# Optimization experiments

Measured on AMD Instinct MI355X. Metric: run time of the kernel, lower is better.

Reference implementation:

```python
import jax, jax.numpy as jnp
import numpy as np

D_MODEL = 256
NUM_UNIVERSES = 8
D_UNIVERSE = D_MODEL // NUM_UNIVERSES
B, S = 1, 1024
TEMP = 5.0
NEG = -1e9


def setup_inputs() -> dict:
    key = jax.random.key(0)
    ks = jax.random.split(key, 5)
    scale = 1.0 / np.sqrt(D_MODEL)
    return {
        "x": jax.random.normal(ks[0], (B, S, D_MODEL), dtype=jnp.float32),
        "Wq": jax.random.normal(ks[1], (D_MODEL, D_MODEL), dtype=jnp.float32) * scale,
        "bq": jnp.zeros((D_MODEL,), dtype=jnp.float32),
        "Wk": jax.random.normal(ks[2], (D_MODEL, D_MODEL), dtype=jnp.float32) * scale,
        "bk": jnp.zeros((D_MODEL,), dtype=jnp.float32),
        "Wv": jax.random.normal(ks[3], (D_MODEL, D_MODEL), dtype=jnp.float32) * scale,
        "bv": jnp.zeros((D_MODEL,), dtype=jnp.float32),
        "Wo": jax.random.normal(ks[4], (D_MODEL, D_MODEL), dtype=jnp.float32) * scale,
        "bo": jnp.zeros((D_MODEL,), dtype=jnp.float32),
    }


def reference(x, Wq, bq, Wk, bk, Wv, bv, Wo, bo):
    b, s, d = x.shape
    h, du = NUM_UNIVERSES, D_UNIVERSE
    # Projections; Q,K squashed to [0,1] fuzzy truth values
    Q = jax.nn.sigmoid(x @ Wq + bq)
    K = jax.nn.sigmoid(x @ Wk + bk)
    V = x @ Wv + bv
    # [B,S,D] -> [B,H,S,du]
    Q = Q.reshape(b, s, h, du).transpose(0, 2, 1, 3)
    K = K.reshape(b, s, h, du).transpose(0, 2, 1, 3)
    V = V.reshape(b, s, h, du).transpose(0, 2, 1, 3)
    # Fuzzy implication: clamp(1 - Q_i + K_j, max=1), mean over d_universe
    # Broadcast to [B,H,S,S,du] (the memory-heavy intermediate)
    implication = jnp.minimum(1.0 - Q[:, :, :, None, :] + K[:, :, None, :, :], 1.0)
    truth = implication.mean(axis=-1)  # [B,H,S,S]
    # Causal mask
    causal = jnp.tril(jnp.ones((s, s), dtype=bool))
    truth = jnp.where(causal[None, None], truth, NEG)
    attn = jax.nn.softmax(truth * TEMP, axis=-1)
    out = jnp.einsum("bhij,bhjd->bhid", attn, V)
    out = out.transpose(0, 2, 1, 3).reshape(b, s, d)
    return out @ Wo + bo
```

## Files before the change

### kernel.cpp

```cpp
#include <hip/hip_runtime.h>
#include <hip/hip_bf16.h>
#include <math.h>

#define S_LEN 1024
#define DM    256
#define DU    32
#define TEMPF 5.0f
#define NS    4

typedef float    f32x4  __attribute__((ext_vector_type(4)));
typedef short    bf16x8 __attribute__((ext_vector_type(8)));
typedef _Float16 f16x2  __attribute__((ext_vector_type(2)));
typedef _Float16 f16x8  __attribute__((ext_vector_type(8)));

__device__ __forceinline__ unsigned short f32_to_bf16_rne(float x) {
    unsigned int b = __float_as_uint(x);
    b += 0x7FFFu + ((b >> 16) & 1u);
    return (unsigned short)(b >> 16);
}

__device__ __forceinline__ void split_bf16(float f, unsigned short& h, unsigned short& l) {
    h = f32_to_bf16_rne(f);
    float hf = __uint_as_float((unsigned int)h << 16);
    l = f32_to_bf16_rne(f - hf);
}

__global__ __launch_bounds__(256) void qkv_proj_kernel(
    const float* __restrict__ x,
    const float* __restrict__ Wq, const float* __restrict__ bq,
    const float* __restrict__ Wk, const float* __restrict__ bk,
    const float* __restrict__ Wv, const float* __restrict__ bv,
    float* __restrict__ qo, float* __restrict__ ko, float* __restrict__ vo)
{
    const int n0g = blockIdx.x * 64;
    const int mat = n0g >> 8;
    const int n0  = n0g & 255;
    const float* __restrict__ W    = (mat == 0) ? Wq : ((mat == 1) ? Wk : Wv);
    const float* __restrict__ bias = (mat == 0) ? bq : ((mat == 1) ? bk : bv);
    float* __restrict__ dst        = (mat == 0) ? qo : ((mat == 1) ? ko : vo);

    const int m0   = blockIdx.y * 64;
    const int t    = threadIdx.x;
    const int w    = t >> 6;
    const int lane = t & 63;
    const int fm   = lane & 15;
    const int quad = lane >> 4;
    const int q8   = quad * 8;

    __shared__ __align__(16) unsigned short Ah[2][64][40], Al[2][64][40];
    __shared__ __align__(16) unsigned short Bh[2][64][40], Bl[2][64][40];

    const int xr  = t >> 2;
    const int xf  = (t & 3) * 8;
    const int wn  = t & 63;
    const int wkc = (t >> 6) * 8;

    f32x4 acc[4];
    #pragma unroll
    for (int nt = 0; nt < 4; nt++)
        #pragma unroll
        for (int i = 0; i < 4; i++) acc[nt][i] = 0.0f;

    const float* xbase = x + (m0 + xr) * DM + xf;
    float xa[8], wv[8];

    {
        float4 a0 = *(const float4*)xbase;
        float4 a1 = *(const float4*)(xbase + 4);
        xa[0]=a0.x; xa[1]=a0.y; xa[2]=a0.z; xa[3]=a0.w;
        xa[4]=a1.x; xa[5]=a1.y; xa[6]=a1.z; xa[7]=a1.w;
        #pragma unroll
        for (int i = 0; i < 8; i++) wv[i] = W[(wkc + i) * DM + n0 + wn];
    }
    {
        bf16x8 vh, vl;
        #pragma unroll
        for (int i = 0; i < 8; i++) { unsigned short h,l; split_bf16(xa[i],h,l); vh[i]=(short)h; vl[i]=(short)l; }
        *(bf16x8*)&Ah[0][xr][xf] = vh; *(bf16x8*)&Al[0][xr][xf] = vl;
        #pragma unroll
        for (int i = 0; i < 8; i++) { unsigned short h,l; split_bf16(wv[i],h,l); vh[i]=(short)h; vl[i]=(short)l; }
        *(bf16x8*)&Bh[0][wn][wkc] = vh; *(bf16x8*)&Bl[0][wn][wkc] = vl;
    }
    __syncthreads();

    int buf = 0;
    for (int step = 0; step < 8; step++) {
        if (step < 7) {
            const float* xp = xbase + (step + 1) * 32;
            float4 a0 = *(const float4*)xp;
            float4 a1 = *(const float4*)(xp + 4);
            xa[0]=a0.x; xa[1]=a0.y; xa[2]=a0.z; xa[3]=a0.w;
            xa[4]=a1.x; xa[5]=a1.y; xa[6]=a1.z; xa[7]=a1.w;
            #pragma unroll
            for (int i = 0; i < 8; i++)
                wv[i] = W[((step + 1) * 32 + wkc + i) * DM + n0 + wn];
        }
        {
            bf16x8 ah = *(const bf16x8*)&Ah[buf][16 * w + fm][q8];
            bf16x8 al = *(const bf16x8*)&Al[buf][16 * w + fm][q8];
            #pragma unroll
            for (int nt = 0; nt < 4; nt++) {
                bf16x8 bh = *(const bf16x8*)&Bh[buf][nt * 16 + fm][q8];
                bf16x8 bl = *(const bf16x8*)&Bl[buf][nt * 16 + fm][q8];
                acc[nt] = __builtin_amdgcn_mfma_f32_16x16x32_bf16(ah, bh, acc[nt], 0, 0, 0);
                acc[nt] = __builtin_amdgcn_mfma_f32_16x16x32_bf16(al, bh, acc[nt], 0, 0, 0);
                acc[nt] = __builtin_amdgcn_mfma_f32_16x16x32_bf16(ah, bl, acc[nt], 0, 0, 0);
            }
        }
        if (step < 7) {
            const int nb = buf ^ 1;
            bf16x8 vh, vl;
            #pragma unroll
            for (int i = 0; i < 8; i++) { unsigned short h,l; split_bf16(xa[i],h,l); vh[i]=(short)h; vl[i]=(short)l; }
            *(bf16x8*)&Ah[nb][xr][xf] = vh; *(bf16x8*)&Al[nb][xr][xf] = vl;
            #pragma unroll
            for (int i = 0; i < 8; i++) { unsigned short h,l; split_bf16(wv[i],h,l); vh[i]=(short)h; vl[i]=(short)l; }
            *(bf16x8*)&Bh[nb][wn][wkc] = vh; *(bf16x8*)&Bl[nb][wn][wkc] = vl;
            __syncthreads();
            buf = nb;
        }
    }

    #pragma unroll
    for (int nt = 0; nt < 4; nt++) {
        const int col = n0 + nt * 16 + fm;
        const float bb = bias[col];
        const int hh = col >> 5;
        const int dd = col & 31;
        float* dp = dst + hh * (S_LEN * DU) + dd;
        #pragma unroll
        for (int reg = 0; reg < 4; reg++) {
            const int row = m0 + 16 * w + quad * 4 + reg;
            float val = acc[nt][reg] + bb;
            if (mat < 2) val = 1.0f / (1.0f + __expf(-val));
            dp[row * DU] = val;
        }
    }
}

__global__ __launch_bounds__(256, 2) void attn_kernel(
    const float* __restrict__ q, const float* __restrict__ k,
    const float* __restrict__ v,
    float* __restrict__ part_o, float* __restrict__ part_l)
{
    const int bid = blockIdx.x;
    const int it4 = 15 - (bid >> 5);
    const int sub = bid & 31;
    const int h   = sub & 7;
    const int s   = sub >> 3;
    const int t   = threadIdx.x;
    const int r   = t >> 4;
    const int c   = t & 15;
    const int w   = t >> 6;
    const int i0  = it4 * 64;

    __shared__ __align__(16) _Float16       Kh[64][40];
    __shared__ __align__(16) unsigned short Vt[32][88];
    __shared__ __align__(16) unsigned short Ps[64][88];

    f16x2 qh[4][16];
    #pragma unroll
    for (int kq = 0; kq < 4; kq++) {
        const float* qrow = q + h * (S_LEN * DU) + (i0 + r + 16 * kq) * DU;
        #pragma unroll
        for (int d4 = 0; d4 < 8; d4++) {
            float4 qv = *(const float4*)&qrow[d4 * 4];
            qh[kq][d4*2+0] = (f16x2){(_Float16)qv.x, (_Float16)qv.y};
            qh[kq][d4*2+1] = (f16x2){(_Float16)qv.z, (_Float16)qv.w};
        }
    }
    const f16x2 one2  = {(_Float16)1.0f, (_Float16)1.0f};
    const f16x2 zero2 = {(_Float16)0.0f, (_Float16)0.0f};

    float lpart[4] = {0.0f, 0.0f, 0.0f, 0.0f};
    f32x4 acc0 = {0.0f, 0.0f, 0.0f, 0.0f};
    f32x4 acc1 = {0.0f, 0.0f, 0.0f, 0.0f};

    const int jr = t >> 2;
    const int d0 = (t & 3) * 8;
    const float* kbase = k + h * (S_LEN * DU);
    const float* vbase = v + h * (S_LEN * DU);

    const int lane = t & 63;
    const int m    = lane & 15;
    const int quad = lane >> 4;

    const int njt = it4 + 1;
    float4 ka, kb, va, vb;
    if (s < njt) {
        const float* kp = kbase + (s * 64 + jr) * DU + d0;
        const float* vp = vbase + (s * 64 + jr) * DU + d0;
        ka = *(const float4*)kp; kb = *(const float4*)(kp + 4);
        va = *(const float4*)vp; vb = *(const float4*)(vp + 4);
    }

    for (int jt = s; jt < njt; jt += NS) {
        __syncthreads();
        {
            float kv[8] = {ka.x, ka.y, ka.z, ka.w, kb.x, kb.y, kb.z, kb.w};
            f16x8 kh8;
            #pragma unroll
            for (int i = 0; i < 8; i++) kh8[i] = (_Float16)kv[i];
            *(f16x8*)&Kh[jr][d0] = kh8;
            float vv[8] = {va.x, va.y, va.z, va.w, vb.x, vb.y, vb.z, vb.w};
            #pragma unroll
            for (int i = 0; i < 8; i++)
                Vt[d0 + i][jr] = f32_to_bf16_rne(vv[i]);
        }
        __syncthreads();
        if (jt + NS < njt) {
            const float* kp = kbase + ((jt + NS) * 64 + jr) * DU + d0;
            const float* vp = vbase + ((jt + NS) * 64 + jr) * DU + d0;
            ka = *(const float4*)kp; kb = *(const float4*)(kp + 4);
            va = *(const float4*)vp; vb = *(const float4*)(vp + 4);
        }

        #pragma unroll
        for (int q4 = 0; q4 < 4; q4++) {
            const int jj  = c + q4 * 16;
            const int jgl = jt * 64 + jj;
            float sacc[4] = {0.0f, 0.0f, 0.0f, 0.0f};
            #pragma unroll
            for (int d8 = 0; d8 < 4; d8++) {
                f16x8 k8 = *(const f16x8*)&Kh[jj][d8 * 8];
                #pragma unroll
                for (int p2 = 0; p2 < 4; p2++) {
                    f16x2 kk = {k8[2*p2], k8[2*p2+1]};
                    #pragma unroll
                    for (int kq = 0; kq < 4; kq++) {
                        f16x2 diff = qh[kq][d8*4+p2] - kk;
                        f16x2 mx = __builtin_elementwise_max(diff, zero2);
#if defined(__has_builtin) && __has_builtin(__builtin_amdgcn_fdot2)
                        sacc[kq] = __builtin_amdgcn_fdot2(mx, one2, sacc[kq], false);
#else
                        sacc[kq] += (float)mx[0] + (float)mx[1];
#endif
                    }
                }
            }
            #pragma unroll
            for (int kq = 0; kq < 4; kq++) {
                const int ig = i0 + r + 16 * kq;
                const float p = (jgl <= ig)
                    ? __expf(TEMPF - (TEMPF / 32.0f) * sacc[kq]) : 0.0f;
                lpart[kq] += p;
                Ps[r + 16 * kq][jj] = f32_to_bf16_rne(p);
            }
        }
        __syncthreads();

        #pragma unroll
        for (int kc = 0; kc < 2; kc++) {
            bf16x8 a  = *(const bf16x8*)&Ps[16 * w + m][kc * 32 + quad * 8];
            bf16x8 b0 = *(const bf16x8*)&Vt[m]     [kc * 32 + quad * 8];
            bf16x8 b1 = *(const bf16x8*)&Vt[m + 16][kc * 32 + quad * 8];
            acc0 = __builtin_amdgcn_mfma_f32_16x16x32_bf16(a, b0, acc0, 0, 0, 0);
            acc1 = __builtin_amdgcn_mfma_f32_16x16x32_bf16(a, b1, acc1, 0, 0, 0);
        }
    }

    #pragma unroll
    for (int off = 8; off; off >>= 1)
        #pragma unroll
        for (int kq = 0; kq < 4; kq++)
            lpart[kq] += __shfl_xor(lpart[kq], off, 16);

    const int pbase = (h * 16 + it4) * NS + s;
    float* po = part_o + (size_t)pbase * 2048;
    #pragma unroll
    for (int reg = 0; reg < 4; reg++) {
        const int row = 16 * w + quad * 4 + reg;
        po[row * 32 + m]      = acc0[reg];
        po[row * 32 + m + 16] = acc1[reg];
    }
    if (c == 0) {
        #pragma unroll
        for (int kq = 0; kq < 4; kq++)
            part_l[pbase * 64 + r + 16 * kq] = lpart[kq];
    }
}

__global__ __launch_bounds__(256) void out_proj_kernel(
    const float* __restrict__ part_o, const float* __restrict__ part_l,
    const float* __restrict__ W, const float* __restrict__ bias,
    float* __restrict__ dst)
{
    const int n0  = blockIdx.x * 32;
    const int it4 = blockIdx.y;
    const int m0  = it4 * 64;
    const int t    = threadIdx.x;
    const int w    = t >> 6;
    const int lane = t & 63;
    const int fm   = lane & 15;
    const int quad = lane >> 4;
    const int q8   = quad * 8;

    __shared__ __align__(16) unsigned short Ah[2][64][40], Al[2][64][40];
    __shared__ __align__(16) unsigned short Bh[2][32][40], Bl[2][32][40];

    const int xr  = t >> 2;
    const int xf  = (t & 3) * 8;
    const int wn  = t & 31;
    const int wkb = (t >> 5) * 4;

    f32x4 acc[2];
    #pragma unroll
    for (int nt = 0; nt < 2; nt++)
        #pragma unroll
        for (int i = 0; i < 4; i++) acc[nt][i] = 0.0f;

    float xa[8], wv[4];

    auto loadA = [&](int h) {
        const int base = (h * 16 + it4) * NS;
        float o[8] = {0,0,0,0,0,0,0,0};
        float l = 0.0f;
        #pragma unroll
        for (int s2 = 0; s2 < NS; s2++) {
            const float* po = part_o + (size_t)(base + s2) * 2048 + xr * 32 + xf;
            float4 p0 = *(const float4*)po;
            float4 p1 = *(const float4*)(po + 4);
            o[0]+=p0.x; o[1]+=p0.y; o[2]+=p0.z; o[3]+=p0.w;
            o[4]+=p1.x; o[5]+=p1.y; o[6]+=p1.z; o[7]+=p1.w;
            l += part_l[(base + s2) * 64 + xr];
        }
        const float inv = 1.0f / l;
        #pragma unroll
        for (int i = 0; i < 8; i++) xa[i] = o[i] * inv;
    };
    auto loadW = [&](int k0) {
        #pragma unroll
        for (int i = 0; i < 4; i++) wv[i] = W[(k0 + wkb + i) * DM + n0 + wn];
    };
    auto storeT = [&](int b) {
        bf16x8 vh, vl;
        #pragma unroll
        for (int i = 0; i < 8; i++) { unsigned short h,l; split_bf16(xa[i],h,l); vh[i]=(short)h; vl[i]=(short)l; }
        *(bf16x8*)&Ah[b][xr][xf] = vh; *(bf16x8*)&Al[b][xr][xf] = vl;
        ushort4 bh4, bl4;
        unsigned short hh, ll;
        split_bf16(wv[0], hh, ll); bh4.x = hh; bl4.x = ll;
        split_bf16(wv[1], hh, ll); bh4.y = hh; bl4.y = ll;
        split_bf16(wv[2], hh, ll); bh4.z = hh; bl4.z = ll;
        split_bf16(wv[3], hh, ll); bh4.w = hh; bl4.w = ll;
        *(ushort4*)&Bh[b][wn][wkb] = bh4;
        *(ushort4*)&Bl[b][wn][wkb] = bl4;
    };

    loadA(0); loadW(0);
    storeT(0);
    __syncthreads();

    int buf = 0;
    for (int step = 0; step < 8; step++) {
        if (step < 7) { loadA(step + 1); loadW((step + 1) * 32); }
        {
            bf16x8 ah = *(const bf16x8*)&Ah[buf][16 * w + fm][q8];
            bf16x8 al = *(const bf16x8*)&Al[buf][16 * w + fm][q8];
            #pragma unroll
            for (int nt = 0; nt < 2; nt++) {
                bf16x8 bh = *(const bf16x8*)&Bh[buf][nt * 16 + fm][q8];
                bf16x8 bl = *(const bf16x8*)&Bl[buf][nt * 16 + fm][q8];
                acc[nt] = __builtin_amdgcn_mfma_f32_16x16x32_bf16(ah, bh, acc[nt], 0, 0, 0);
                acc[nt] = __builtin_amdgcn_mfma_f32_16x16x32_bf16(al, bh, acc[nt], 0, 0, 0);
                acc[nt] = __builtin_amdgcn_mfma_f32_16x16x32_bf16(ah, bl, acc[nt], 0, 0, 0);
            }
        }
        if (step < 7) {
            const int nb = buf ^ 1;
            storeT(nb);
            __syncthreads();
            buf = nb;
        }
    }

    #pragma unroll
    for (int nt = 0; nt < 2; nt++) {
        const int col = n0 + nt * 16 + fm;
        const float bb = bias[col];
        #pragma unroll
        for (int reg = 0; reg < 4; reg++) {
            const int row = m0 + 16 * w + quad * 4 + reg;
            dst[row * DM + col] = acc[nt][reg] + bb;
        }
    }
}

extern "C" void kernel_launch(void* const* d_in, const int* in_sizes, int n_in,
                              void* d_out, int out_size, void* d_ws, size_t ws_size,
                              hipStream_t stream)
{
    const float* x  = (const float*)d_in[0];
    const float* Wq = (const float*)d_in[1];
    const float* bq = (const float*)d_in[2];
    const float* Wk = (const float*)d_in[3];
    const float* bk = (const float*)d_in[4];
    const float* Wv = (const float*)d_in[5];
    const float* bv = (const float*)d_in[6];
    const float* Wo = (const float*)d_in[7];
    const float* bo = (const float*)d_in[8];
    float* out = (float*)d_out;

    float* ws      = (float*)d_ws;
    float* q       = ws;
    float* k       = q + 262144;
    float* v       = k + 262144;
    float* part_o  = v + 262144;
    float* part_l  = part_o + 1048576;

    qkv_proj_kernel<<<dim3(12, 16), 256, 0, stream>>>(x, Wq, bq, Wk, bk, Wv, bv, q, k, v);
    attn_kernel<<<dim3(512), 256, 0, stream>>>(q, k, v, part_o, part_l);
    out_proj_kernel<<<dim3(8, 16), 256, 0, stream>>>(part_o, part_l, Wo, bo, out);
}
```

Measured before the change: 107.1 us.

## Rebalance causal attention split-K and halve projection tiles for more blocks

The attention kernel now splits long causal row tiles (it4 >= 8) across 8 KV-splits instead of 4, so the grid grows from 512 to 768 blocks and the longest blocks get shorter, and occupancy is raised to 3 blocks per CU. The QKV and output projection kernels use 32-row tiles, doubling their block counts so more CUs have work. The output reduction reads a variable number of partials per row tile, and the workspace for partials grows. The trade-off is more partial writes and reduction traffic plus smaller per-block MFMA work.

```diff
diff --git a/kernel.cpp b/kernel.cpp
--- a/kernel.cpp
+++ b/kernel.cpp
@@ -6,13 +6,15 @@
 #define DM    256
 #define DU    32
 #define TEMPF 5.0f
-#define NS    4
 
 typedef float    f32x4  __attribute__((ext_vector_type(4)));
 typedef short    bf16x8 __attribute__((ext_vector_type(8)));
 typedef _Float16 f16x2  __attribute__((ext_vector_type(2)));
 typedef _Float16 f16x8  __attribute__((ext_vector_type(8)));
 
+__device__ __host__ inline int task_cnt(int it4)  { return it4 < 8 ? 4 : 8; }
+__device__ __host__ inline int task_base(int it4) { return it4 < 8 ? it4 * 4 : 32 + (it4 - 8) * 8; }
+
 __device__ __forceinline__ unsigned short f32_to_bf16_rne(float x) {
     unsigned int b = __float_as_uint(x);
     b += 0x7FFFu + ((b >> 16) & 1u);
@@ -25,7 +27,7 @@
     l = f32_to_bf16_rne(f - hf);
 }
 
-__global__ __launch_bounds__(256) void qkv_proj_kernel(
+__global__ __launch_bounds__(256, 2) void qkv_proj_kernel(
     const float* __restrict__ x,
     const float* __restrict__ Wq, const float* __restrict__ bq,
     const float* __restrict__ Wk, const float* __restrict__ bk,
@@ -39,69 +41,70 @@
     const float* __restrict__ bias = (mat == 0) ? bq : ((mat == 1) ? bk : bv);
     float* __restrict__ dst        = (mat == 0) ? qo : ((mat == 1) ? ko : vo);
 
-    const int m0   = blockIdx.y * 64;
+    const int m0   = blockIdx.y * 32;
     const int t    = threadIdx.x;
     const int w    = t >> 6;
     const int lane = t & 63;
     const int fm   = lane & 15;
     const int quad = lane >> 4;
     const int q8   = quad * 8;
-
-    __shared__ __align__(16) unsigned short Ah[2][64][40], Al[2][64][40];
+    const int mh   = w & 1;
+    const int nb2  = (w >> 1) * 2;
+
+    __shared__ __align__(16) unsigned short Ah[2][32][40], Al[2][32][40];
     __shared__ __align__(16) unsigned short Bh[2][64][40], Bl[2][64][40];
 
-    const int xr  = t >> 2;
-    const int xf  = (t & 3) * 8;
+    const int xr  = t >> 3;
+    const int xf  = (t & 7) * 4;
     const int wn  = t & 63;
     const int wkc = (t >> 6) * 8;
 
-    f32x4 acc[4];
+    f32x4 acc[2];
     #pragma unroll
-    for (int nt = 0; nt < 4; nt++)
+    for (int nt = 0; nt < 2; nt++)
         #pragma unroll
         for (int i = 0; i < 4; i++) acc[nt][i] = 0.0f;
 
     const float* xbase = x + (m0 + xr) * DM + xf;
-    float xa[8], wv[8];
-
-    {
-        float4 a0 = *(const float4*)xbase;
-        float4 a1 = *(const float4*)(xbase + 4);
+    float xa[4], wv[8];
+
+    auto loadX = [&](int k0) {
+        float4 a0 = *(const float4*)(xbase + k0);
         xa[0]=a0.x; xa[1]=a0.y; xa[2]=a0.z; xa[3]=a0.w;
-        xa[4]=a1.x; xa[5]=a1.y; xa[6]=a1.z; xa[7]=a1.w;
-        #pragma unroll
-        for (int i = 0; i < 8; i++) wv[i] = W[(wkc + i) * DM + n0 + wn];
-    }
-    {
+    };
+    auto loadW = [&](int k0) {
+        #pragma unroll
+        for (int i = 0; i < 8; i++) wv[i] = W[(k0 + wkc + i) * DM + n0 + wn];
+    };
+    auto storeT = [&](int b) {
+        ushort4 ah4, al4;
+        unsigned short hh, ll;
+        split_bf16(xa[0], hh, ll); ah4.x = hh; al4.x = ll;
+        split_bf16(xa[1], hh, ll); ah4.y = hh; al4.y = ll;
+        split_bf16(xa[2], hh, ll); ah4.z = hh; al4.z = ll;
+        split_bf16(xa[3], hh, ll); ah4.w = hh; al4.w = ll;
+        *(ushort4*)&Ah[b][xr][xf] = ah4;
+        *(ushort4*)&Al[b][xr][xf] = al4;
         bf16x8 vh, vl;
         #pragma unroll
-        for (int i = 0; i < 8; i++) { unsigned short h,l; split_bf16(xa[i],h,l); vh[i]=(short)h; vl[i]=(short)l; }
-        *(bf16x8*)&Ah[0][xr][xf] = vh; *(bf16x8*)&Al[0][xr][xf] = vl;
-        #pragma unroll
-        for (int i = 0; i < 8; i++) { unsigned short h,l; split_bf16(wv[i],h,l); vh[i]=(short)h; vl[i]=(short)l; }
-        *(bf16x8*)&Bh[0][wn][wkc] = vh; *(bf16x8*)&Bl[0][wn][wkc] = vl;
-    }
+        for (int i = 0; i < 8; i++) { unsigned short h2,l2; split_bf16(wv[i],h2,l2); vh[i]=(short)h2; vl[i]=(short)l2; }
+        *(bf16x8*)&Bh[b][wn][wkc] = vh; *(bf16x8*)&Bl[b][wn][wkc] = vl;
+    };
+
+    loadX(0); loadW(0);
+    storeT(0);
     __syncthreads();
 
     int buf = 0;
     for (int step = 0; step < 8; step++) {
-        if (step < 7) {
-            const float* xp = xbase + (step + 1) * 32;
-            float4 a0 = *(const float4*)xp;
-            float4 a1 = *(const float4*)(xp + 4);
-            xa[0]=a0.x; xa[1]=a0.y; xa[2]=a0.z; xa[3]=a0.w;
-            xa[4]=a1.x; xa[5]=a1.y; xa[6]=a1.z; xa[7]=a1.w;
+        if (step < 7) { loadX((step + 1) * 32); loadW((step + 1) * 32); }
+        {
+            bf16x8 ah = *(const bf16x8*)&Ah[buf][16 * mh + fm][q8];
+            bf16x8 al = *(const bf16x8*)&Al[buf][16 * mh + fm][q8];
             #pragma unroll
-            for (int i = 0; i < 8; i++)
-                wv[i] = W[((step + 1) * 32 + wkc + i) * DM + n0 + wn];
-        }
-        {
-            bf16x8 ah = *(const bf16x8*)&Ah[buf][16 * w + fm][q8];
-            bf16x8 al = *(const bf16x8*)&Al[buf][16 * w + fm][q8];
-            #pragma unroll
-            for (int nt = 0; nt < 4; nt++) {
-                bf16x8 bh = *(const bf16x8*)&Bh[buf][nt * 16 + fm][q8];
-                bf16x8 bl = *(const bf16x8*)&Bl[buf][nt * 16 + fm][q8];
+            for (int nt = 0; nt < 2; nt++) {
+                bf16x8 bh = *(const bf16x8*)&Bh[buf][(nb2 + nt) * 16 + fm][q8];
+                bf16x8 bl = *(const bf16x8*)&Bl[buf][(nb2 + nt) * 16 + fm][q8];
                 acc[nt] = __builtin_amdgcn_mfma_f32_16x16x32_bf16(ah, bh, acc[nt], 0, 0, 0);
                 acc[nt] = __builtin_amdgcn_mfma_f32_16x16x32_bf16(al, bh, acc[nt], 0, 0, 0);
                 acc[nt] = __builtin_amdgcn_mfma_f32_16x16x32_bf16(ah, bl, acc[nt], 0, 0, 0);
@@ -109,28 +112,22 @@
         }
         if (step < 7) {
             const int nb = buf ^ 1;
-            bf16x8 vh, vl;
-            #pragma unroll
-            for (int i = 0; i < 8; i++) { unsigned short h,l; split_bf16(xa[i],h,l); vh[i]=(short)h; vl[i]=(short)l; }
-            *(bf16x8*)&Ah[nb][xr][xf] = vh; *(bf16x8*)&Al[nb][xr][xf] = vl;
-            #pragma unroll
-            for (int i = 0; i < 8; i++) { unsigned short h,l; split_bf16(wv[i],h,l); vh[i]=(short)h; vl[i]=(short)l; }
-            *(bf16x8*)&Bh[nb][wn][wkc] = vh; *(bf16x8*)&Bl[nb][wn][wkc] = vl;
+            storeT(nb);
             __syncthreads();
             buf = nb;
         }
     }
 
     #pragma unroll
-    for (int nt = 0; nt < 4; nt++) {
-        const int col = n0 + nt * 16 + fm;
+    for (int nt = 0; nt < 2; nt++) {
+        const int col = n0 + (nb2 + nt) * 16 + fm;
         const float bb = bias[col];
         const int hh = col >> 5;
         const int dd = col & 31;
         float* dp = dst + hh * (S_LEN * DU) + dd;
         #pragma unroll
         for (int reg = 0; reg < 4; reg++) {
-            const int row = m0 + 16 * w + quad * 4 + reg;
+            const int row = m0 + 16 * mh + quad * 4 + reg;
             float val = acc[nt][reg] + bb;
             if (mat < 2) val = 1.0f / (1.0f + __expf(-val));
             dp[row * DU] = val;
@@ -138,16 +135,17 @@
     }
 }
 
-__global__ __launch_bounds__(256, 2) void attn_kernel(
+__global__ __launch_bounds__(256, 3) void attn_kernel(
     const float* __restrict__ q, const float* __restrict__ k,
     const float* __restrict__ v,
     float* __restrict__ part_o, float* __restrict__ part_l)
 {
     const int bid = blockIdx.x;
-    const int it4 = 15 - (bid >> 5);
-    const int sub = bid & 31;
-    const int h   = sub & 7;
-    const int s   = sub >> 3;
+    const int h   = bid / 96;
+    const int rm  = bid - h * 96;
+    int it4, s, NSi;
+    if (rm < 32) { it4 = rm >> 2;        s = rm & 3;         NSi = 4; }
+    else         { it4 = 8 + ((rm - 32) >> 3); s = (rm - 32) & 7; NSi = 8; }
     const int t   = threadIdx.x;
     const int r   = t >> 4;
     const int c   = t & 15;
@@ -194,7 +192,7 @@
         va = *(const float4*)vp; vb = *(const float4*)(vp + 4);
     }
 
-    for (int jt = s; jt < njt; jt += NS) {
+    for (int jt = s; jt < njt; jt += NSi) {
         __syncthreads();
         {
             float kv[8] = {ka.x, ka.y, ka.z, ka.w, kb.x, kb.y, kb.z, kb.w};
@@ -208,9 +206,9 @@
                 Vt[d0 + i][jr] = f32_to_bf16_rne(vv[i]);
         }
         __syncthreads();
-        if (jt + NS < njt) {
-            const float* kp = kbase + ((jt + NS) * 64 + jr) * DU + d0;
-            const float* vp = vbase + ((jt + NS) * 64 + jr) * DU + d0;
+        if (jt + NSi < njt) {
+            const float* kp = kbase + ((jt + NSi) * 64 + jr) * DU + d0;
+            const float* vp = vbase + ((jt + NSi) * 64 + jr) * DU + d0;
             ka = *(const float4*)kp; kb = *(const float4*)(kp + 4);
             va = *(const float4*)vp; vb = *(const float4*)(vp + 4);
         }
@@ -265,7 +263,7 @@
         for (int kq = 0; kq < 4; kq++)
             lpart[kq] += __shfl_xor(lpart[kq], off, 16);
 
-    const int pbase = (h * 16 + it4) * NS + s;
+    const int pbase = h * 96 + task_base(it4) + s;
     float* po = part_o + (size_t)pbase * 2048;
     #pragma unroll
     for (int reg = 0; reg < 4; reg++) {
@@ -280,71 +278,71 @@
     }
 }
 
-__global__ __launch_bounds__(256) void out_proj_kernel(
+__global__ __launch_bounds__(256, 2) void out_proj_kernel(
     const float* __restrict__ part_o, const float* __restrict__ part_l,
     const float* __restrict__ W, const float* __restrict__ bias,
     float* __restrict__ dst)
 {
-    const int n0  = blockIdx.x * 32;
-    const int it4 = blockIdx.y;
-    const int m0  = it4 * 64;
+    const int n0   = blockIdx.x * 32;
+    const int m0   = blockIdx.y * 32;
+    const int it4  = m0 >> 6;
+    const int half = m0 & 32;
     const int t    = threadIdx.x;
     const int w    = t >> 6;
     const int lane = t & 63;
     const int fm   = lane & 15;
     const int quad = lane >> 4;
     const int q8   = quad * 8;
-
-    __shared__ __align__(16) unsigned short Ah[2][64][40], Al[2][64][40];
+    const int mh   = w & 1;
+    const int nh   = w >> 1;
+
+    __shared__ __align__(16) unsigned short Ah[2][32][40], Al[2][32][40];
     __shared__ __align__(16) unsigned short Bh[2][32][40], Bl[2][32][40];
 
-    const int xr  = t >> 2;
-    const int xf  = (t & 3) * 8;
+    const int xr  = t >> 3;
+    const int xf  = (t & 7) * 4;
     const int wn  = t & 31;
     const int wkb = (t >> 5) * 4;
 
-    f32x4 acc[2];
-    #pragma unroll
-    for (int nt = 0; nt < 2; nt++)
-        #pragma unroll
-        for (int i = 0; i < 4; i++) acc[nt][i] = 0.0f;
-
-    float xa[8], wv[4];
+    f32x4 acc = {0.0f, 0.0f, 0.0f, 0.0f};
+    float xa[4], wv[4];
+
+    const int cnt  = task_cnt(it4);
+    const int tb   = task_base(it4);
 
     auto loadA = [&](int h) {
-        const int base = (h * 16 + it4) * NS;
-        float o[8] = {0,0,0,0,0,0,0,0};
+        const int base = h * 96 + tb;
+        float o[4] = {0,0,0,0};
         float l = 0.0f;
-        #pragma unroll
-        for (int s2 = 0; s2 < NS; s2++) {
-            const float* po = part_o + (size_t)(base + s2) * 2048 + xr * 32 + xf;
+        for (int s2 = 0; s2 < cnt; s2++) {
+            const float* po = part_o + (size_t)(base + s2) * 2048 + (half + xr) * 32 + xf;
             float4 p0 = *(const float4*)po;
-            float4 p1 = *(const float4*)(po + 4);
             o[0]+=p0.x; o[1]+=p0.y; o[2]+=p0.z; o[3]+=p0.w;
-            o[4]+=p1.x; o[5]+=p1.y; o[6]+=p1.z; o[7]+=p1.w;
-            l += part_l[(base + s2) * 64 + xr];
+            l += part_l[(base + s2) * 64 + half + xr];
         }
         const float inv = 1.0f / l;
         #pragma unroll
-        for (int i = 0; i < 8; i++) xa[i] = o[i] * inv;
+        for (int i = 0; i < 4; i++) xa[i] = o[i] * inv;
     };
     auto loadW = [&](int k0) {
         #pragma unroll
         for (int i = 0; i < 4; i++) wv[i] = W[(k0 + wkb + i) * DM + n0 + wn];
     };
     auto storeT = [&](int b) {
-        bf16x8 vh, vl;
-        #pragma unroll
-        for (int i = 0; i < 8; i++) { unsigned short h,l; split_bf16(xa[i],h,l); vh[i]=(short)h; vl[i]=(short)l; }
-        *(bf16x8*)&Ah[b][xr][xf] = vh; *(bf16x8*)&Al[b][xr][xf] = vl;
-        ushort4 bh4, bl4;
+        ushort4 h4, l4;
         unsigned short hh, ll;
-        split_bf16(wv[0], hh, ll); bh4.x = hh; bl4.x = ll;
-        split_bf16(wv[1], hh, ll); bh4.y = hh; bl4.y = ll;
-        split_bf16(wv[2], hh, ll); bh4.z = hh; bl4.z = ll;
-        split_bf16(wv[3], hh, ll); bh4.w = hh; bl4.w = ll;
-        *(ushort4*)&Bh[b][wn][wkb] = bh4;
-        *(ushort4*)&Bl[b][wn][wkb] = bl4;
+        split_bf16(xa[0], hh, ll); h4.x = hh; l4.x = ll;
+        split_bf16(xa[1], hh, ll); h4.y = hh; l4.y = ll;
+        split_bf16(xa[2], hh, ll); h4.z = hh; l4.z = ll;
+        split_bf16(xa[3], hh, ll); h4.w = hh; l4.w = ll;
+        *(ushort4*)&Ah[b][xr][xf] = h4;
+        *(ushort4*)&Al[b][xr][xf] = l4;
+        split_bf16(wv[0], hh, ll); h4.x = hh; l4.x = ll;
+        split_bf16(wv[1], hh, ll); h4.y = hh; l4.y = ll;
+        split_bf16(wv[2], hh, ll); h4.z = hh; l4.z = ll;
+        split_bf16(wv[3], hh, ll); h4.w = hh; l4.w = ll;
+        *(ushort4*)&Bh[b][wn][wkb] = h4;
+        *(ushort4*)&Bl[b][wn][wkb] = l4;
     };
 
     loadA(0); loadW(0);
@@ -355,16 +353,13 @@
     for (int step = 0; step < 8; step++) {
         if (step < 7) { loadA(step + 1); loadW((step + 1) * 32); }
         {
-            bf16x8 ah = *(const bf16x8*)&Ah[buf][16 * w + fm][q8];
-            bf16x8 al = *(const bf16x8*)&Al[buf][16 * w + fm][q8];
-            #pragma unroll
-            for (int nt = 0; nt < 2; nt++) {
-                bf16x8 bh = *(const bf16x8*)&Bh[buf][nt * 16 + fm][q8];
-                bf16x8 bl = *(const bf16x8*)&Bl[buf][nt * 16 + fm][q8];
-                acc[nt] = __builtin_amdgcn_mfma_f32_16x16x32_bf16(ah, bh, acc[nt], 0, 0, 0);
-                acc[nt] = __builtin_amdgcn_mfma_f32_16x16x32_bf16(al, bh, acc[nt], 0, 0, 0);
-                acc[nt] = __builtin_amdgcn_mfma_f32_16x16x32_bf16(ah, bl, acc[nt], 0, 0, 0);
-            }
+            bf16x8 ah = *(const bf16x8*)&Ah[buf][16 * mh + fm][q8];
+            bf16x8 al = *(const bf16x8*)&Al[buf][16 * mh + fm][q8];
+            bf16x8 bh = *(const bf16x8*)&Bh[buf][16 * nh + fm][q8];
+            bf16x8 bl = *(const bf16x8*)&Bl[buf][16 * nh + fm][q8];
+            acc = __builtin_amdgcn_mfma_f32_16x16x32_bf16(ah, bh, acc, 0, 0, 0);
+            acc = __builtin_amdgcn_mfma_f32_16x16x32_bf16(al, bh, acc, 0, 0, 0);
+            acc = __builtin_amdgcn_mfma_f32_16x16x32_bf16(ah, bl, acc, 0, 0, 0);
         }
         if (step < 7) {
             const int nb = buf ^ 1;
@@ -374,14 +369,13 @@
         }
     }
 
-    #pragma unroll
-    for (int nt = 0; nt < 2; nt++) {
-        const int col = n0 + nt * 16 + fm;
+    {
+        const int col = n0 + 16 * nh + fm;
         const float bb = bias[col];
         #pragma unroll
         for (int reg = 0; reg < 4; reg++) {
-            const int row = m0 + 16 * w + quad * 4 + reg;
-            dst[row * DM + col] = acc[nt][reg] + bb;
+            const int row = m0 + 16 * mh + quad * 4 + reg;
+            dst[row * DM + col] = acc[reg] + bb;
         }
     }
 }
@@ -406,9 +400,9 @@
     float* k       = q + 262144;
     float* v       = k + 262144;
     float* part_o  = v + 262144;
-    float* part_l  = part_o + 1048576;
-
-    qkv_proj_kernel<<<dim3(12, 16), 256, 0, stream>>>(x, Wq, bq, Wk, bk, Wv, bv, q, k, v);
-    attn_kernel<<<dim3(512), 256, 0, stream>>>(q, k, v, part_o, part_l);
-    out_proj_kernel<<<dim3(8, 16), 256, 0, stream>>>(part_o, part_l, Wo, bo, out);
-}
+    float* part_l  = part_o + 1572864;
+
+    qkv_proj_kernel<<<dim3(12, 32), 256, 0, stream>>>(x, Wq, bq, Wk, bk, Wv, bv, q, k, v);
+    attn_kernel<<<dim3(768), 256, 0, stream>>>(q, k, v, part_o, part_l);
+    out_proj_kernel<<<dim3(8, 32), 256, 0, stream>>>(part_o, part_l, Wo, bo, out);
+}
```

After: 118.2 us. 10.4% more time.
